# Performance work log

Measured on AMD Instinct MI355X. Metric: run time of the kernel, lower is better.

The kernel has to match this reference:

```python
import jax, jax.numpy as jnp
import numpy as np

B, N, F_IN, E_DIM, F, T = 4, 64, 32, 32, 64, 3


def setup_inputs() -> dict:
    key = jax.random.key(0)
    ks = jax.random.split(key, 8)
    X = jax.random.normal(ks[0], (B, N, F_IN), jnp.float32)
    # adjacency mask over the dense N*N ordered-pair layout, broadcast dim 1
    A = (jax.random.uniform(ks[1], (B, N * N, 1)) < 0.25).astype(jnp.float32)
    E = jax.random.normal(ks[2], (B, N * N, E_DIM), jnp.float32)

    def glorot(k, shape):
        fan_in, fan_out = shape
        lim = np.sqrt(6.0 / (fan_in + fan_out)).astype(np.float32)
        return jax.random.uniform(k, shape, jnp.float32, -lim, lim)

    W_embed = glorot(ks[3], (F_IN, F))
    b_embed = jnp.zeros((F,), jnp.float32)
    W_edge = glorot(ks[4], (E_DIM, F * F))
    b_edge = jnp.zeros((F * F,), jnp.float32)
    gru_k = glorot(ks[5], (F, 3 * F))        # input kernel  [F, 3F] (z|r|h)
    gru_rk = glorot(ks[6], (F, 3 * F))       # recurrent kernel
    gru_b = jnp.zeros((3 * F,), jnp.float32)   # input bias
    gru_rb = jnp.zeros((3 * F,), jnp.float32)  # recurrent bias (reset_after)
    return {"X": X, "A": A, "E": E, "W_embed": W_embed, "b_embed": b_embed,
            "W_edge": W_edge, "b_edge": b_edge, "gru_k": gru_k,
            "gru_rk": gru_rk, "gru_b": gru_b, "gru_rb": gru_rb}


def _gru_step(h, x, Wk, Uk, b, rb):
    # Keras GRU cell, reset_after=True: gate order z, r, h
    xg = x @ Wk + b
    hg = h @ Uk + rb
    xz, xr, xh = jnp.split(xg, 3, axis=-1)
    hz, hr, hh = jnp.split(hg, 3, axis=-1)
    z = jax.nn.sigmoid(xz + hz)
    r = jax.nn.sigmoid(xr + hr)
    cand = jnp.tanh(xh + r * hh)
    return z * h + (1.0 - z) * cand


def reference(X, A, E, W_embed, b_embed, W_edge, b_edge,
              gru_k, gru_rk, gru_b, gru_rb):
    H = jax.nn.relu(X @ W_embed + b_embed)            # [B,N,F]
    mask = A.reshape(B, N, N, 1)                      # adjacency mask
    # per-edge transformation matrices (E is constant across T rounds,
    # so the edge MLP is hoisted out of the loop -- same math as original)
    Amat = jax.nn.relu(E @ W_edge + b_edge).reshape(B, N, N, F, F)
    for _ in range(T):
        # message for target i from source j: A_{ij} @ H_j  (batched matvec)
        msgs = jnp.einsum('bnmij,bmj->bnmi', Amat, H)  # [B,N,N,F]
        agg = jnp.sum(msgs * mask, axis=2)             # [B,N,F]
        # GRU over the length-2 sequence [old_state, agg_messages], h0 = 0
        h = jnp.zeros_like(H)
        h = _gru_step(h, H, gru_k, gru_rk, gru_b, gru_rb)
        H = _gru_step(h, agg, gru_k, gru_rk, gru_b, gru_rb)
    return H
```

## Files before the change

### kernel.cpp

```cpp
#include <hip/hip_runtime.h>
#include <math.h>

#define Bv   4
#define Nv   64
#define FIN  32
#define EDIM 32
#define Fv   64
#define NN   (Nv*Nv)
#define ZROW 256

typedef __bf16 bf16x8 __attribute__((ext_vector_type(8)));
typedef float  f32x4  __attribute__((ext_vector_type(4)));

__device__ __forceinline__ float sigmoidf_(float x) {
    return 1.f / (1.f + __expf(-x));
}

__global__ __launch_bounds__(64) void prep_kernel(
    const float* __restrict__ X, const float* __restrict__ W_embed,
    const float* __restrict__ b_embed, const float* __restrict__ A,
    const float* __restrict__ E, const float* __restrict__ W_edge,
    float* __restrict__ H0, float* __restrict__ H1,
    __bf16* __restrict__ Wf, __bf16* __restrict__ Ebf,
    int* __restrict__ ml_g, int* __restrict__ cnt_g)
{
    const int blk  = blockIdx.x;
    const int lane = threadIdx.x;

    if (blk < 256) {
        const int nt = blk;
        const int kb = (lane >> 4) * 8;
        const int c  = nt*16 + (lane & 15);
        bf16x8 v;
        #pragma unroll
        for (int t = 0; t < 8; ++t)
            v[t] = (__bf16)W_edge[(kb + t)*4096 + c];
        *(bf16x8*)(Wf + ((size_t)(nt*64 + lane))*8) = v;
        if (blk == 0) {
            H0[ZROW*Fv + lane] = 0.f;
            H1[ZROW*Fv + lane] = 0.f;
        }
    } else if (blk < 512) {
        const int bn = blk - 256;
        const int b  = bn >> 6;
        const int n  = bn & 63;
        __shared__ int ml[Nv];
        __shared__ int cnt_s;
        if (lane == 0) {
            int c = 0;
            const float* arow = A + b*NN + n*Nv;
            for (int m = 0; m < Nv; ++m)
                if (arow[m] != 0.f) ml[c++] = m;
            cnt_s = c;
        }
        __syncthreads();
        const int cnt = cnt_s;
        ml_g[bn*64 + lane] = (lane < cnt) ? (b*Nv + ml[lane]) : ZROW;
        if (lane == 0) cnt_g[bn] = cnt;
        __bf16 row[EDIM];
        if (lane < cnt) {
            const float* er = E + ((size_t)(b*NN + n*Nv + ml[lane]))*EDIM;
            #pragma unroll
            for (int t = 0; t < 8; ++t) {
                const float4 x = *(const float4*)(er + 4*t);
                row[4*t  ] = (__bf16)x.x; row[4*t+1] = (__bf16)x.y;
                row[4*t+2] = (__bf16)x.z; row[4*t+3] = (__bf16)x.w;
            }
        } else {
            #pragma unroll
            for (int e = 0; e < EDIM; ++e) row[e] = (__bf16)0.f;
        }
        __bf16* dst = Ebf + ((size_t)(bn*64 + lane))*EDIM;
        #pragma unroll
        for (int t = 0; t < 4; ++t)
            *(bf16x8*)(dst + 8*t) = *(bf16x8*)(row + 8*t);
    } else {
        const int bn = blk - 512;
        __shared__ float xs[FIN];
        if (lane < FIN) xs[lane] = X[bn*FIN + lane];
        __syncthreads();
        float acc = b_embed[lane];
        #pragma unroll
        for (int k = 0; k < FIN; ++k)
            acc = fmaf(xs[k], W_embed[k*Fv + lane], acc);
        H0[bn*Fv + lane] = fmaxf(acc, 0.f);
    }
}

template<int MTN>
__device__ __forceinline__ void msg_body(
    int bn, int qq, int w, int lane,
    const float* __restrict__ Hin, const __bf16* __restrict__ Wf,
    const float* __restrict__ b_edge, const __bf16* __restrict__ Ebf,
    const int* __restrict__ ml_g, float* __restrict__ agg_g)
{
    const int c16 = lane & 15;
    const int rg  = (lane >> 4) * 4;
    const int kb  = (lane >> 4) * 8;

    bf16x8 af[MTN];
    int4   ri[MTN];
    #pragma unroll
    for (int mt = 0; mt < MTN; ++mt) {
        af[mt] = *(const bf16x8*)(Ebf + ((size_t)(bn*64 + mt*16 + c16))*EDIM + kb);
        ri[mt] = *(const int4*)(ml_g + bn*64 + mt*16 + rg);
    }

    const int i0 = qq*8 + w*2;
    float p0 = 0.f, p1 = 0.f;

    #pragma unroll
    for (int u = 0; u < 4; ++u) {
        const int jc = u*16 + c16;
        float hu[MTN][4];
        #pragma unroll
        for (int mt = 0; mt < MTN; ++mt) {
            hu[mt][0] = Hin[ri[mt].x*Fv + jc];
            hu[mt][1] = Hin[ri[mt].y*Fv + jc];
            hu[mt][2] = Hin[ri[mt].z*Fv + jc];
            hu[mt][3] = Hin[ri[mt].w*Fv + jc];
        }
        #pragma unroll
        for (int ii = 0; ii < 2; ++ii) {
            const int nt = (i0 + ii)*4 + u;
            const bf16x8 bf = *(const bf16x8*)(Wf + ((size_t)(nt*64 + lane))*8);
            const float  be = b_edge[nt*16 + c16];
            f32x4 cb; cb[0] = be; cb[1] = be; cb[2] = be; cb[3] = be;
            float acc = 0.f;
            #pragma unroll
            for (int mt = 0; mt < MTN; ++mt) {
                f32x4 d = __builtin_amdgcn_mfma_f32_16x16x32_bf16(af[mt], bf, cb, 0, 0, 0);
                acc = fmaf(fmaxf(d[0], 0.f), hu[mt][0], acc);
                acc = fmaf(fmaxf(d[1], 0.f), hu[mt][1], acc);
                acc = fmaf(fmaxf(d[2], 0.f), hu[mt][2], acc);
                acc = fmaf(fmaxf(d[3], 0.f), hu[mt][3], acc);
            }
            if (ii == 0) p0 += acc; else p1 += acc;
        }
    }
    #pragma unroll
    for (int off = 32; off > 0; off >>= 1) {
        p0 += __shfl_xor(p0, off);
        p1 += __shfl_xor(p1, off);
    }
    if (lane == 0) {
        agg_g[bn*Fv + i0]     = p0;
        agg_g[bn*Fv + i0 + 1] = p1;
    }
}

__global__ __launch_bounds__(256) void msg_kernel(
    const float* __restrict__ Hin, const __bf16* __restrict__ Wf,
    const float* __restrict__ b_edge, const __bf16* __restrict__ Ebf,
    const int* __restrict__ ml_g, const int* __restrict__ cnt_g,
    float* __restrict__ agg_g)
{
    const int bn   = blockIdx.x;
    const int qq   = blockIdx.y;
    const int tid  = threadIdx.x;
    const int w    = tid >> 6;
    const int lane = tid & 63;

    const int cnt = cnt_g[bn];
    const int Mt  = (cnt == 0) ? 1 : ((cnt + 15) >> 4);

    if (Mt <= 1) {
        msg_body<1>(bn, qq, w, lane, Hin, Wf, b_edge, Ebf, ml_g, agg_g);
    } else if (Mt == 2) {
        msg_body<2>(bn, qq, w, lane, Hin, Wf, b_edge, Ebf, ml_g, agg_g);
    } else {
        const int c16 = lane & 15;
        const int rg  = (lane >> 4) * 4;
        const int kb  = (lane >> 4) * 8;
        const int i0  = qq*8 + w*2;
        #pragma unroll
        for (int ii = 0; ii < 2; ++ii) {
            float part = 0.f;
            #pragma unroll 1
            for (int u = 0; u < 4; ++u) {
                const int jc = u*16 + c16;
                const int nt = (i0 + ii)*4 + u;
                const bf16x8 bf = *(const bf16x8*)(Wf + ((size_t)(nt*64 + lane))*8);
                const float  be = b_edge[nt*16 + c16];
                f32x4 cb; cb[0] = be; cb[1] = be; cb[2] = be; cb[3] = be;
                for (int mt = 0; mt < Mt; ++mt) {
                    const bf16x8 a_ = *(const bf16x8*)(Ebf + ((size_t)(bn*64 + mt*16 + c16))*EDIM + kb);
                    const int4 ri = *(const int4*)(ml_g + bn*64 + mt*16 + rg);
                    f32x4 d = __builtin_amdgcn_mfma_f32_16x16x32_bf16(a_, bf, cb, 0, 0, 0);
                    part = fmaf(fmaxf(d[0], 0.f), Hin[ri.x*Fv + jc], part);
                    part = fmaf(fmaxf(d[1], 0.f), Hin[ri.y*Fv + jc], part);
                    part = fmaf(fmaxf(d[2], 0.f), Hin[ri.z*Fv + jc], part);
                    part = fmaf(fmaxf(d[3], 0.f), Hin[ri.w*Fv + jc], part);
                }
            }
            #pragma unroll
            for (int off = 32; off > 0; off >>= 1)
                part += __shfl_xor(part, off);
            if (lane == 0) agg_g[bn*Fv + i0 + ii] = part;
        }
    }
}

__global__ __launch_bounds__(192) void gru_kernel(
    const float* __restrict__ Hin, const float* __restrict__ agg_g,
    float* __restrict__ Hout,
    const float* __restrict__ gk, const float* __restrict__ grk,
    const float* __restrict__ gb, const float* __restrict__ grb)
{
    const int bn  = blockIdx.x;
    const int tid = threadIdx.x;

    __shared__ float h_old[Fv];
    __shared__ float aggs[Fv];
    __shared__ float h1[Fv];
    __shared__ float xg[3*Fv];
    __shared__ float hg[3*Fv];

    if (tid < Fv) {
        h_old[tid] = Hin[bn*Fv + tid];
        aggs[tid]  = agg_g[bn*Fv + tid];
    }
    __syncthreads();

    {
        float a0 = 0.f, a1 = 0.f, a2 = 0.f, a3 = 0.f;
        #pragma unroll
        for (int k = 0; k < 16; ++k) {
            a0 = fmaf(h_old[k],      gk[(k     )*192 + tid], a0);
            a1 = fmaf(h_old[k + 16], gk[(k + 16)*192 + tid], a1);
            a2 = fmaf(h_old[k + 32], gk[(k + 32)*192 + tid], a2);
            a3 = fmaf(h_old[k + 48], gk[(k + 48)*192 + tid], a3);
        }
        xg[tid] = gb[tid] + ((a0 + a1) + (a2 + a3));
    }
    __syncthreads();
    if (tid < Fv) {
        float z    = sigmoidf_(xg[tid]       + grb[tid]);
        float r    = sigmoidf_(xg[64 + tid]  + grb[64 + tid]);
        float cand = tanhf    (xg[128 + tid] + r * grb[128 + tid]);
        h1[tid] = (1.f - z) * cand;
    }
    __syncthreads();

    {
        float x0 = 0.f, x1 = 0.f, x2 = 0.f, x3 = 0.f;
        float y0 = 0.f, y1 = 0.f, y2 = 0.f, y3 = 0.f;
        #pragma unroll
        for (int k = 0; k < 16; ++k) {
            x0 = fmaf(aggs[k],      gk [(k     )*192 + tid], x0);
            x1 = fmaf(aggs[k + 16], gk [(k + 16)*192 + tid], x1);
            x2 = fmaf(aggs[k + 32], gk [(k + 32)*192 + tid], x2);
            x3 = fmaf(aggs[k + 48], gk [(k + 48)*192 + tid], x3);
            y0 = fmaf(h1[k],        grk[(k     )*192 + tid], y0);
            y1 = fmaf(h1[k + 16],   grk[(k + 16)*192 + tid], y1);
            y2 = fmaf(h1[k + 32],   grk[(k + 32)*192 + tid], y2);
            y3 = fmaf(h1[k + 48],   grk[(k + 48)*192 + tid], y3);
        }
        xg[tid] = gb[tid]  + ((x0 + x1) + (x2 + x3));
        hg[tid] = grb[tid] + ((y0 + y1) + (y2 + y3));
    }
    __syncthreads();
    if (tid < Fv) {
        float z    = sigmoidf_(xg[tid]       + hg[tid]);
        float r    = sigmoidf_(xg[64 + tid]  + hg[64 + tid]);
        float cand = tanhf    (xg[128 + tid] + r * hg[128 + tid]);
        Hout[bn*Fv + tid] = z * h1[tid] + (1.f - z) * cand;
    }
}

extern "C" void kernel_launch(void* const* d_in, const int* in_sizes, int n_in,
                              void* d_out, int out_size, void* d_ws, size_t ws_size,
                              hipStream_t stream)
{
    const float* X       = (const float*)d_in[0];
    const float* A       = (const float*)d_in[1];
    const float* E       = (const float*)d_in[2];
    const float* W_embed = (const float*)d_in[3];
    const float* b_embed = (const float*)d_in[4];
    const float* W_edge  = (const float*)d_in[5];
    const float* b_edge  = (const float*)d_in[6];
    const float* gk      = (const float*)d_in[7];
    const float* grk     = (const float*)d_in[8];
    const float* gb      = (const float*)d_in[9];
    const float* grb     = (const float*)d_in[10];
    float* out = (float*)d_out;

    float*  H0  = (float*)d_ws;
    float*  H1  = H0 + (ZROW + 1)*Fv;
    __bf16* Wf  = (__bf16*)(H1 + (ZROW + 1)*Fv);
    __bf16* Ebf = Wf + 256*64*8;
    int*    ml_g  = (int*)(Ebf + (size_t)Bv*Nv*64*EDIM);
    int*    cnt_g = ml_g + Bv*Nv*64;

    const dim3 mgrid(Bv*Nv, 8);

    prep_kernel<<<768, 64, 0, stream>>>(X, W_embed, b_embed, A, E, W_edge,
                                        H0, H1, Wf, Ebf, ml_g, cnt_g);

    msg_kernel<<<mgrid, 256, 0, stream>>>(H0, Wf, b_edge, Ebf, ml_g, cnt_g, out);
    gru_kernel<<<Bv*Nv, 192, 0, stream>>>(H0, out, H1, gk, grk, gb, grb);
    msg_kernel<<<mgrid, 256, 0, stream>>>(H1, Wf, b_edge, Ebf, ml_g, cnt_g, out);
    gru_kernel<<<Bv*Nv, 192, 0, stream>>>(H1, out, H0, gk, grk, gb, grb);
    msg_kernel<<<mgrid, 256, 0, stream>>>(H0, Wf, b_edge, Ebf, ml_g, cnt_g, H1);
    gru_kernel<<<Bv*Nv, 192, 0, stream>>>(H0, H1, out, gk, grk, gb, grb);
}
```

Before: 48.56 us.

## Fuse message and GRU kernels into one per-round kernel with LDS aggregates

Merges the message-aggregation kernel and the GRU kernel into a single round kernel, so each round needs one launch instead of two. The aggregate vector now stays in shared memory rather than going through global memory. Each block now handles all 64 output features of a node, looping over 8 pairs per wave, where before the work was split across 8 blocks in grid y. This cuts the grid from 2048 blocks to 256 blocks, which lowers parallelism and lengthens the serial per-block message work.

```diff
diff --git a/kernel.cpp b/kernel.cpp
--- a/kernel.cpp
+++ b/kernel.cpp
@@ -88,11 +88,11 @@
 }
 
 template<int MTN>
-__device__ __forceinline__ void msg_body(
-    int bn, int qq, int w, int lane,
+__device__ __forceinline__ void msg_phase(
+    int bn, int w, int lane,
     const float* __restrict__ Hin, const __bf16* __restrict__ Wf,
     const float* __restrict__ b_edge, const __bf16* __restrict__ Ebf,
-    const int* __restrict__ ml_g, float* __restrict__ agg_g)
+    const int* __restrict__ ml_g, float* __restrict__ agg_lds)
 {
     const int c16 = lane & 15;
     const int rg  = (lane >> 4) * 4;
@@ -106,80 +106,93 @@
         ri[mt] = *(const int4*)(ml_g + bn*64 + mt*16 + rg);
     }
 
-    const int i0 = qq*8 + w*2;
-    float p0 = 0.f, p1 = 0.f;
-
-    #pragma unroll
-    for (int u = 0; u < 4; ++u) {
-        const int jc = u*16 + c16;
-        float hu[MTN][4];
-        #pragma unroll
-        for (int mt = 0; mt < MTN; ++mt) {
-            hu[mt][0] = Hin[ri[mt].x*Fv + jc];
-            hu[mt][1] = Hin[ri[mt].y*Fv + jc];
-            hu[mt][2] = Hin[ri[mt].z*Fv + jc];
-            hu[mt][3] = Hin[ri[mt].w*Fv + jc];
-        }
-        #pragma unroll
-        for (int ii = 0; ii < 2; ++ii) {
-            const int nt = (i0 + ii)*4 + u;
-            const bf16x8 bf = *(const bf16x8*)(Wf + ((size_t)(nt*64 + lane))*8);
-            const float  be = b_edge[nt*16 + c16];
-            f32x4 cb; cb[0] = be; cb[1] = be; cb[2] = be; cb[3] = be;
-            float acc = 0.f;
+    #pragma unroll 1
+    for (int s2 = 0; s2 < 8; ++s2) {
+        const int i0 = w*16 + s2*2;
+        float p0 = 0.f, p1 = 0.f;
+
+        #pragma unroll
+        for (int u = 0; u < 4; ++u) {
+            const int jc = u*16 + c16;
+            float hu[MTN][4];
             #pragma unroll
             for (int mt = 0; mt < MTN; ++mt) {
-                f32x4 d = __builtin_amdgcn_mfma_f32_16x16x32_bf16(af[mt], bf, cb, 0, 0, 0);
-                acc = fmaf(fmaxf(d[0], 0.f), hu[mt][0], acc);
-                acc = fmaf(fmaxf(d[1], 0.f), hu[mt][1], acc);
-                acc = fmaf(fmaxf(d[2], 0.f), hu[mt][2], acc);
-                acc = fmaf(fmaxf(d[3], 0.f), hu[mt][3], acc);
-            }
-            if (ii == 0) p0 += acc; else p1 += acc;
-        }
-    }
-    #pragma unroll
-    for (int off = 32; off > 0; off >>= 1) {
-        p0 += __shfl_xor(p0, off);
-        p1 += __shfl_xor(p1, off);
-    }
-    if (lane == 0) {
-        agg_g[bn*Fv + i0]     = p0;
-        agg_g[bn*Fv + i0 + 1] = p1;
-    }
-}
-
-__global__ __launch_bounds__(256) void msg_kernel(
-    const float* __restrict__ Hin, const __bf16* __restrict__ Wf,
-    const float* __restrict__ b_edge, const __bf16* __restrict__ Ebf,
-    const int* __restrict__ ml_g, const int* __restrict__ cnt_g,
-    float* __restrict__ agg_g)
+                hu[mt][0] = Hin[ri[mt].x*Fv + jc];
+                hu[mt][1] = Hin[ri[mt].y*Fv + jc];
+                hu[mt][2] = Hin[ri[mt].z*Fv + jc];
+                hu[mt][3] = Hin[ri[mt].w*Fv + jc];
+            }
+            #pragma unroll
+            for (int ii = 0; ii < 2; ++ii) {
+                const int nt = (i0 + ii)*4 + u;
+                const bf16x8 bf = *(const bf16x8*)(Wf + ((size_t)(nt*64 + lane))*8);
+                const float  be = b_edge[nt*16 + c16];
+                f32x4 cb; cb[0] = be; cb[1] = be; cb[2] = be; cb[3] = be;
+                float acc = 0.f;
+                #pragma unroll
+                for (int mt = 0; mt < MTN; ++mt) {
+                    f32x4 d = __builtin_amdgcn_mfma_f32_16x16x32_bf16(af[mt], bf, cb, 0, 0, 0);
+                    acc = fmaf(fmaxf(d[0], 0.f), hu[mt][0], acc);
+                    acc = fmaf(fmaxf(d[1], 0.f), hu[mt][1], acc);
+                    acc = fmaf(fmaxf(d[2], 0.f), hu[mt][2], acc);
+                    acc = fmaf(fmaxf(d[3], 0.f), hu[mt][3], acc);
+                }
+                if (ii == 0) p0 += acc; else p1 += acc;
+            }
+        }
+        #pragma unroll
+        for (int off = 32; off > 0; off >>= 1) {
+            p0 += __shfl_xor(p0, off);
+            p1 += __shfl_xor(p1, off);
+        }
+        if (lane == 0) {
+            agg_lds[i0]     = p0;
+            agg_lds[i0 + 1] = p1;
+        }
+    }
+}
+
+__global__ __launch_bounds__(256) void round_kernel(
+    const float* __restrict__ Hin, float* __restrict__ Hout,
+    const __bf16* __restrict__ Wf, const float* __restrict__ b_edge,
+    const __bf16* __restrict__ Ebf, const int* __restrict__ ml_g,
+    const int* __restrict__ cnt_g,
+    const float* __restrict__ gk, const float* __restrict__ grk,
+    const float* __restrict__ gb, const float* __restrict__ grb)
 {
     const int bn   = blockIdx.x;
-    const int qq   = blockIdx.y;
     const int tid  = threadIdx.x;
     const int w    = tid >> 6;
     const int lane = tid & 63;
 
+    __shared__ float aggs[Fv];
+    __shared__ float h_old[Fv];
+    __shared__ float h1[Fv];
+    __shared__ float xg[3*Fv];
+    __shared__ float hg[3*Fv];
+
+    if (tid < Fv) h_old[tid] = Hin[bn*Fv + tid];
+    __syncthreads();
+
     const int cnt = cnt_g[bn];
     const int Mt  = (cnt == 0) ? 1 : ((cnt + 15) >> 4);
 
     if (Mt <= 1) {
-        msg_body<1>(bn, qq, w, lane, Hin, Wf, b_edge, Ebf, ml_g, agg_g);
+        msg_phase<1>(bn, w, lane, Hin, Wf, b_edge, Ebf, ml_g, aggs);
     } else if (Mt == 2) {
-        msg_body<2>(bn, qq, w, lane, Hin, Wf, b_edge, Ebf, ml_g, agg_g);
+        msg_phase<2>(bn, w, lane, Hin, Wf, b_edge, Ebf, ml_g, aggs);
     } else {
         const int c16 = lane & 15;
         const int rg  = (lane >> 4) * 4;
         const int kb  = (lane >> 4) * 8;
-        const int i0  = qq*8 + w*2;
-        #pragma unroll
-        for (int ii = 0; ii < 2; ++ii) {
+        #pragma unroll 1
+        for (int s = 0; s < 16; ++s) {
+            const int i = w*16 + s;
             float part = 0.f;
             #pragma unroll 1
             for (int u = 0; u < 4; ++u) {
                 const int jc = u*16 + c16;
-                const int nt = (i0 + ii)*4 + u;
+                const int nt = i*4 + u;
                 const bf16x8 bf = *(const bf16x8*)(Wf + ((size_t)(nt*64 + lane))*8);
                 const float  be = b_edge[nt*16 + c16];
                 f32x4 cb; cb[0] = be; cb[1] = be; cb[2] = be; cb[3] = be;
@@ -196,33 +209,12 @@
             #pragma unroll
             for (int off = 32; off > 0; off >>= 1)
                 part += __shfl_xor(part, off);
-            if (lane == 0) agg_g[bn*Fv + i0 + ii] = part;
-        }
-    }
-}
-
-__global__ __launch_bounds__(192) void gru_kernel(
-    const float* __restrict__ Hin, const float* __restrict__ agg_g,
-    float* __restrict__ Hout,
-    const float* __restrict__ gk, const float* __restrict__ grk,
-    const float* __restrict__ gb, const float* __restrict__ grb)
-{
-    const int bn  = blockIdx.x;
-    const int tid = threadIdx.x;
-
-    __shared__ float h_old[Fv];
-    __shared__ float aggs[Fv];
-    __shared__ float h1[Fv];
-    __shared__ float xg[3*Fv];
-    __shared__ float hg[3*Fv];
-
-    if (tid < Fv) {
-        h_old[tid] = Hin[bn*Fv + tid];
-        aggs[tid]  = agg_g[bn*Fv + tid];
-    }
-    __syncthreads();
-
-    {
+            if (lane == 0) aggs[i] = part;
+        }
+    }
+    __syncthreads();
+
+    if (tid < 3*Fv) {
         float a0 = 0.f, a1 = 0.f, a2 = 0.f, a3 = 0.f;
         #pragma unroll
         for (int k = 0; k < 16; ++k) {
@@ -242,7 +234,7 @@
     }
     __syncthreads();
 
-    {
+    if (tid < 3*Fv) {
         float x0 = 0.f, x1 = 0.f, x2 = 0.f, x3 = 0.f;
         float y0 = 0.f, y1 = 0.f, y2 = 0.f, y3 = 0.f;
         #pragma unroll
@@ -292,15 +284,13 @@
     int*    ml_g  = (int*)(Ebf + (size_t)Bv*Nv*64*EDIM);
     int*    cnt_g = ml_g + Bv*Nv*64;
 
-    const dim3 mgrid(Bv*Nv, 8);
-
     prep_kernel<<<768, 64, 0, stream>>>(X, W_embed, b_embed, A, E, W_edge,
                                         H0, H1, Wf, Ebf, ml_g, cnt_g);
 
-    msg_kernel<<<mgrid, 256, 0, stream>>>(H0, Wf, b_edge, Ebf, ml_g, cnt_g, out);
-    gru_kernel<<<Bv*Nv, 192, 0, stream>>>(H0, out, H1, gk, grk, gb, grb);
-    msg_kernel<<<mgrid, 256, 0, stream>>>(H1, Wf, b_edge, Ebf, ml_g, cnt_g, out);
-    gru_kernel<<<Bv*Nv, 192, 0, stream>>>(H1, out, H0, gk, grk, gb, grb);
-    msg_kernel<<<mgrid, 256, 0, stream>>>(H0, Wf, b_edge, Ebf, ml_g, cnt_g, H1);
-    gru_kernel<<<Bv*Nv, 192, 0, stream>>>(H0, H1, out, gk, grk, gb, grb);
-}
+    round_kernel<<<Bv*Nv, 256, 0, stream>>>(H0, H1, Wf, b_edge, Ebf, ml_g, cnt_g,
+                                            gk, grk, gb, grb);
+    round_kernel<<<Bv*Nv, 256, 0, stream>>>(H1, H0, Wf, b_edge, Ebf, ml_g, cnt_g,
+                                            gk, grk, gb, grb);
+    round_kernel<<<Bv*Nv, 256, 0, stream>>>(H0, out, Wf, b_edge, Ebf, ml_g, cnt_g,
+                                            gk, grk, gb, grb);
+}
```

Result: slower. 59.54 us (+22.6%).
